# Optimization experiments

Hardware: AMD Instinct MI355X
Metric: run time of the kernel (lower is better)

Reference implementation:

```python
import jax, jax.numpy as jnp
from jax import lax
import numpy as np

H = 128          # hidden_size
E = 300          # embed_dim
V = 100000       # vocab size


def lstm_dir(x, Wih, Whh, b, reverse):
    # x: (B,T,D); Wih: (4H,D); Whh: (4H,H); b: (4H,) (bih+bhh combined)
    B, T, _ = x.shape
    h_dim = Whh.shape[1]
    xg = jnp.einsum('btd,gd->btg', x, Wih) + b  # precompute input gates (B,T,4H)

    def step(carry, xt):
        h, c = carry
        gates = xt + h @ Whh.T
        i, f, g, o = jnp.split(gates, 4, axis=-1)  # PyTorch gate order i,f,g,o
        i = jax.nn.sigmoid(i); f = jax.nn.sigmoid(f)
        g = jnp.tanh(g);       o = jax.nn.sigmoid(o)
        c = f * c + i * g
        h = o * jnp.tanh(c)
        return (h, c), h

    init = (jnp.zeros((B, h_dim), x.dtype), jnp.zeros((B, h_dim), x.dtype))
    _, hs = lax.scan(step, init, jnp.swapaxes(xg, 0, 1), reverse=reverse)
    return jnp.swapaxes(hs, 0, 1)  # (B,T,H)


def bilstm(x, Wih, Whh, b):
    # stacked params: Wih (2,4H,D), Whh (2,4H,H), b (2,4H); dir 0 fwd, dir 1 bwd
    fwd = lstm_dir(x, Wih[0], Whh[0], b[0], False)
    bwd = lstm_dir(x, Wih[1], Whh[1], b[1], True)
    return jnp.concatenate([fwd, bwd], axis=-1)  # (B,T,2H)


def _lstm_params(key, in_dim, h):
    ks = jax.random.split(key, 3)
    s = 1.0 / np.sqrt(h)
    return (jax.random.uniform(ks[0], (2, 4 * h, in_dim), jnp.float32, -s, s),
            jax.random.uniform(ks[1], (2, 4 * h, h), jnp.float32, -s, s),
            jax.random.uniform(ks[2], (2, 4 * h), jnp.float32, -s, s))


def setup_inputs() -> dict:
    key = jax.random.key(0)
    ks = jax.random.split(key, 16)
    inp = {}
    inp['p'] = jax.random.randint(ks[0], (64, 512), 0, V)
    inp['q'] = jax.random.randint(ks[1], (64, 64), 0, V)
    inp['emb'] = jax.random.normal(ks[2], (V, E), jnp.float32) * 0.1
    for name, in_dim, k in [('qenc', E, ks[3]), ('penc', E, ks[4]),
                            ('m1', 8 * H, ks[5]), ('m2', 2 * H, ks[6]),
                            ('out', 2 * H, ks[7])]:
        Wih, Whh, b = _lstm_params(k, in_dim, H)
        inp[name + '_Wih'] = Wih; inp[name + '_Whh'] = Whh; inp[name + '_b'] = b
    inp['att_wc'] = jax.random.normal(ks[8], (2 * H,), jnp.float32) * 0.05
    inp['att_wq'] = jax.random.normal(ks[9], (2 * H,), jnp.float32) * 0.05
    inp['att_wcq'] = jax.random.normal(ks[10], (2 * H,), jnp.float32) * 0.05
    inp['att_b'] = jnp.zeros((), jnp.float32)
    inp['p1_wg'] = jax.random.normal(ks[11], (8 * H,), jnp.float32) * 0.05
    inp['p1_wm'] = jax.random.normal(ks[12], (2 * H,), jnp.float32) * 0.05
    inp['p1_b'] = jnp.zeros((), jnp.float32)
    inp['p2_wg'] = jax.random.normal(ks[13], (8 * H,), jnp.float32) * 0.05
    inp['p2_wm'] = jax.random.normal(ks[14], (2 * H,), jnp.float32) * 0.05
    inp['p2_b'] = jnp.zeros((), jnp.float32)
    return inp


def reference(p, q, emb,
              qenc_Wih, qenc_Whh, qenc_b,
              penc_Wih, penc_Whh, penc_b,
              m1_Wih, m1_Whh, m1_b,
              m2_Wih, m2_Whh, m2_b,
              out_Wih, out_Whh, out_b,
              att_wc, att_wq, att_wcq, att_b,
              p1_wg, p1_wm, p1_b, p2_wg, p2_wm, p2_b):
    q_emb = emb[q]                      # (B,Q,E)
    p_emb = emb[p]                      # (B,C,E)
    qo = bilstm(q_emb, qenc_Wih, qenc_Whh, qenc_b)   # (B,Q,2H)
    co = bilstm(p_emb, penc_Wih, penc_Whh, penc_b)   # (B,C,2H)

    # trilinear similarity (fused form of the original per-q_len loop)
    s = (jnp.einsum('bcd,d->bc', co, att_wc)[:, :, None]
         + jnp.einsum('bqd,d->bq', qo, att_wq)[:, None, :]
         + jnp.einsum('bcd,bqd->bcq', co * att_wcq, qo)
         + att_b)                       # (B,C,Q)
    a = jax.nn.softmax(s, axis=2)
    c2q = jnp.einsum('bcq,bqd->bcd', a, qo)
    bw = jax.nn.softmax(jnp.max(s, axis=2), axis=1)   # (B,C)
    q2c = jnp.einsum('bc,bcd->bd', bw, co)[:, None, :]  # (B,1,2H)
    g = jnp.concatenate([co, c2q, co * c2q, co * q2c], axis=-1)  # (B,C,8H)

    m = bilstm(bilstm(g, m1_Wih, m1_Whh, m1_b), m2_Wih, m2_Whh, m2_b)  # (B,C,2H)
    m2 = bilstm(m, out_Wih, out_Whh, out_b)

    p1_logit = g @ p1_wg + m @ p1_wm + p1_b    # (B,C)
    p2_logit = g @ p2_wg + m2 @ p2_wm + p2_b
    valid = (p != 0)
    p1 = jax.nn.softmax(jnp.where(valid, p1_logit, -jnp.inf), axis=1)
    p2 = jax.nn.softmax(jnp.where(valid, p2_logit, -jnp.inf), axis=1)
    return p1, p2
```

## Files before the change

kernel.cpp:

```cpp
#include <hip/hip_runtime.h>
#include <math.h>
#include <stdint.h>

#define HD    128
#define GATES 512
#define BB    64
#define CL    512
#define QL    64

#define TM 128
#define TN 128
#define TK 32
#define ASTR 40

typedef __attribute__((ext_vector_type(8))) short short8_t;
typedef __attribute__((ext_vector_type(4))) short short4_t;
typedef __attribute__((ext_vector_type(4))) float f32x4;
typedef __attribute__((ext_vector_type(2))) float f32x2;

__device__ __forceinline__ float fast_sigmoid(float x) {
    float e = __builtin_amdgcn_exp2f(-1.44269504f * x);
    return __builtin_amdgcn_rcpf(1.f + e);
}
__device__ __forceinline__ float fast_tanh(float x) {
    float e = __builtin_amdgcn_exp2f(2.88539008f * x);
    float r = __builtin_amdgcn_rcpf(e + 1.f);
    return 1.f - 2.f * r;
}
__device__ __forceinline__ float quad_sum(float v) {
    int y = __builtin_amdgcn_mov_dpp(__float_as_int(v), 0xB1, 0xF, 0xF, 0);
    float s = v + __int_as_float(y);
    int z = __builtin_amdgcn_mov_dpp(__float_as_int(s), 0x4E, 0xF, 0xF, 0);
    return s + __int_as_float(z);
}
#define HPOS(e) ((e) + (((e) >> 5) << 2))

__global__ __launch_bounds__(256)
void splitW_k(const float* __restrict__ W, ushort* __restrict__ P, int K, int Ksp)
{
    int idx = blockIdx.x * 256 + threadIdx.x;
    int per_row = Ksp >> 2;
    int total = 1024 * per_row;
    if (idx >= total) return;
    int row = idx / per_row;
    int c4  = (idx - row * per_row) * 4;

    short4_t o1, o2, o3;
#pragma unroll
    for (int e = 0; e < 4; ++e) {
        int k = c4 + e;
        float x = (k < K) ? W[(size_t)row * K + k] : 0.f;
        uint32_t u1 = __float_as_uint(x) & 0xffff0000u;
        float r1 = x - __uint_as_float(u1);
        uint32_t u2 = __float_as_uint(r1) & 0xffff0000u;
        float r2 = r1 - __uint_as_float(u2);
        uint32_t u3 = __float_as_uint(r2) & 0xffff0000u;
        o1[e] = (short)(u1 >> 16);
        o2[e] = (short)(u2 >> 16);
        o3[e] = (short)(u3 >> 16);
    }
    size_t base = (size_t)row * Ksp + c4;
    size_t ps = (size_t)1024 * Ksp;
    *reinterpret_cast<short4_t*>(&P[base]) = o1;
    *reinterpret_cast<short4_t*>(&P[ps + base]) = o2;
    *reinterpret_cast<short4_t*>(&P[2 * ps + base]) = o3;
}

__global__ __launch_bounds__(256)
void gemm_bf16x3(const float* __restrict__ A, const int* __restrict__ gidx,
                 const ushort* __restrict__ Wpl, const float* __restrict__ bias,
                 float* __restrict__ C, int M, int K, int Ksp)
{
    const int n0   = (blockIdx.x & 3) * TN / 1;
    const int dir  = blockIdx.x >> 2;
    const int m0   = blockIdx.y * TM;
    const int tid  = threadIdx.x;
    const int lane = tid & 63;
    const int wid  = tid >> 6;
    const int wm   = (wid >> 1) * 64;
    const int wn   = (wid & 1) * 64;

    __shared__ __align__(16) ushort As[3][TM * ASTR];
    __shared__ __align__(16) ushort Bs[3][TN * TK];

    const int ar = tid >> 3;
    const int ac = (tid & 7) * 4;

    size_t arow[4];
#pragma unroll
    for (int r = 0; r < 4; ++r) {
        int m = m0 + ar + r * 32;
        arow[r] = gidx ? (size_t)gidx[m] : (size_t)m;
    }

    f32x4 acc[4][4];
#pragma unroll
    for (int i = 0; i < 4; ++i)
#pragma unroll
        for (int j = 0; j < 4; ++j) acc[i][j] = (f32x4)0.f;

    const size_t wps    = (size_t)1024 * Ksp;
    const size_t wdbase = (size_t)dir * 512 * Ksp;

    for (int k0 = 0; k0 < Ksp; k0 += TK) {
#pragma unroll
        for (int r = 0; r < 4; ++r) {
            float4 v = make_float4(0.f, 0.f, 0.f, 0.f);
            if (k0 + ac < K) v = *(const float4*)(A + arow[r] * K + k0 + ac);
            float xs[4] = {v.x, v.y, v.z, v.w};
            short4_t o1, o2, o3;
#pragma unroll
            for (int e = 0; e < 4; ++e) {
                uint32_t u1 = __float_as_uint(xs[e]) & 0xffff0000u;
                float r1 = xs[e] - __uint_as_float(u1);
                uint32_t u2 = __float_as_uint(r1) & 0xffff0000u;
                float r2 = r1 - __uint_as_float(u2);
                uint32_t u3 = __float_as_uint(r2) & 0xffff0000u;
                o1[e] = (short)(u1 >> 16);
                o2[e] = (short)(u2 >> 16);
                o3[e] = (short)(u3 >> 16);
            }
            int wb = (ar + r * 32) * ASTR + ac;
            *reinterpret_cast<short4_t*>(&As[0][wb]) = o1;
            *reinterpret_cast<short4_t*>(&As[1][wb]) = o2;
            *reinterpret_cast<short4_t*>(&As[2][wb]) = o3;
        }
#pragma unroll
        for (int t = 0; t < 6; ++t) {
            int chunk = wid * 6 + t;
            int pl = chunk >> 3;
            int ch = chunk & 7;
            int rrow = ch * 16 + (lane >> 2);
            int ksw  = ((lane & 3) ^ ((rrow >> 1) & 3)) * 8;
            const ushort* src = Wpl + (size_t)pl * wps + wdbase +
                                (size_t)(n0 + rrow) * Ksp + k0 + ksw;
            ushort* dst = &Bs[pl][ch * 512];
            __builtin_amdgcn_global_load_lds(
                reinterpret_cast<const __attribute__((address_space(1))) void*>(
                    reinterpret_cast<uintptr_t>(src)),
                reinterpret_cast<__attribute__((address_space(3))) void*>(
                    reinterpret_cast<uintptr_t>(dst)),
                16, 0, 0);
        }
        __syncthreads();

        const int koff = (lane >> 4) * 8;
        short8_t bf0[4], bf1[4], bf2[4];
#pragma unroll
        for (int j = 0; j < 4; ++j) {
            int nrow = wn + j * 16 + (lane & 15);
            int ks = (((lane >> 4) ^ ((nrow >> 1) & 3)) * 8);
            bf0[j] = *reinterpret_cast<const short8_t*>(&Bs[0][nrow * TK + ks]);
            bf1[j] = *reinterpret_cast<const short8_t*>(&Bs[1][nrow * TK + ks]);
            bf2[j] = *reinterpret_cast<const short8_t*>(&Bs[2][nrow * TK + ks]);
        }
#pragma unroll
        for (int i = 0; i < 4; ++i) {
            int mrow = wm + i * 16 + (lane & 15);
            short8_t a1 = *reinterpret_cast<const short8_t*>(&As[0][mrow * ASTR + koff]);
            short8_t a2 = *reinterpret_cast<const short8_t*>(&As[1][mrow * ASTR + koff]);
            short8_t a3 = *reinterpret_cast<const short8_t*>(&As[2][mrow * ASTR + koff]);
#pragma unroll
            for (int j = 0; j < 4; ++j) {
                f32x4 c = acc[i][j];
                c = __builtin_amdgcn_mfma_f32_16x16x32_bf16(a1, bf0[j], c, 0, 0, 0);
                c = __builtin_amdgcn_mfma_f32_16x16x32_bf16(a1, bf1[j], c, 0, 0, 0);
                c = __builtin_amdgcn_mfma_f32_16x16x32_bf16(a2, bf0[j], c, 0, 0, 0);
                c = __builtin_amdgcn_mfma_f32_16x16x32_bf16(a2, bf1[j], c, 0, 0, 0);
                c = __builtin_amdgcn_mfma_f32_16x16x32_bf16(a1, bf2[j], c, 0, 0, 0);
                c = __builtin_amdgcn_mfma_f32_16x16x32_bf16(a3, bf0[j], c, 0, 0, 0);
                acc[i][j] = c;
            }
        }
        __syncthreads();
    }

    float* Cd = C + (size_t)dir * M * 512;
#pragma unroll
    for (int j = 0; j < 4; ++j) {
        int col = n0 + wn + j * 16 + (lane & 15);
        float bv = bias[dir * 512 + col];
#pragma unroll
        for (int i = 0; i < 4; ++i) {
            int rbase = m0 + wm + i * 16 + ((lane >> 4) << 2);
#pragma unroll
            for (int r = 0; r < 4; ++r)
                Cd[(size_t)(rbase + r) * 512 + col] = acc[i][j][r] + bv;
        }
    }
}

__global__ __launch_bounds__(512) __attribute__((amdgpu_waves_per_eu(2, 2)))
void lstm_dpp(const float* __restrict__ xgP, const float* __restrict__ WhhP,
              float* __restrict__ hoP, int TP,
              const float* __restrict__ xgQ, const float* __restrict__ WhhQ,
              float* __restrict__ hoQ, int TQ)
{
    const int b    = blockIdx.x;
    const int dir  = blockIdx.y;
    const int tid  = threadIdx.x;
    const int l    = tid & 63;
    const int w    = tid >> 6;
    const int u    = w * 16 + (l >> 2);
    const int s    = l & 3;

    const float* xg; const float* Whh; float* ho; int T;
    if (blockIdx.z == 0) { xg = xgP; Whh = WhhP; ho = hoP; T = TP; }
    else                 { xg = xgQ; Whh = WhhQ; ho = hoQ; T = TQ; }

    const float* xgd = xg + (size_t)dir * BB * T * GATES;

    f32x2 wv2[4][16];
#pragma unroll
    for (int g = 0; g < 4; ++g) {
        const float* wr = Whh + ((size_t)dir * GATES + g * 128 + u) * HD + s * 32;
#pragma unroll
        for (int j = 0; j < 8; ++j) {
            float4 t4 = *(const float4*)(wr + j * 4);
            wv2[g][2 * j]     = f32x2{t4.x, t4.y};
            wv2[g][2 * j + 1] = f32x2{t4.z, t4.w};
        }
    }

    __shared__ __align__(16) float hs[2][140];

    if (tid < 140) { hs[0][tid] = 0.f; }
    float c = 0.f;

    int t = dir ? (T - 1) : 0;
    const int dt = dir ? -1 : 1;

    float xc[4], xn[4];
#pragma unroll
    for (int g = 0; g < 4; ++g)
        xc[g] = xgd[((size_t)b * T + t) * GATES + g * 128 + u];

    const int rdbase = HPOS(s * 32);
    __syncthreads();

    for (int step = 0; step < T; ++step) {
        const int tn = t + dt;
        const int rbuf = step & 1, wbuf = rbuf ^ 1;

        if (step + 1 < T) {
#pragma unroll
            for (int g = 0; g < 4; ++g)
                xn[g] = xgd[((size_t)b * T + tn) * GATES + g * 128 + u];
        }

        f32x2 p0 = {0.f, 0.f}, p1 = {0.f, 0.f}, p2 = {0.f, 0.f}, p3 = {0.f, 0.f};
#pragma unroll
        for (int j = 0; j < 8; ++j) {
            float4 h4 = *(const float4*)&hs[rbuf][rdbase + j * 4];
            f32x2 hl = {h4.x, h4.y}, hh = {h4.z, h4.w};
            p0 = __builtin_elementwise_fma(wv2[0][2 * j], hl, p0);
            p1 = __builtin_elementwise_fma(wv2[1][2 * j], hl, p1);
            p2 = __builtin_elementwise_fma(wv2[2][2 * j], hl, p2);
            p3 = __builtin_elementwise_fma(wv2[3][2 * j], hl, p3);
            p0 = __builtin_elementwise_fma(wv2[0][2 * j + 1], hh, p0);
            p1 = __builtin_elementwise_fma(wv2[1][2 * j + 1], hh, p1);
            p2 = __builtin_elementwise_fma(wv2[2][2 * j + 1], hh, p2);
            p3 = __builtin_elementwise_fma(wv2[3][2 * j + 1], hh, p3);
        }
        float pre0 = quad_sum(p0.x + p0.y) + xc[0];
        float pre1 = quad_sum(p1.x + p1.y) + xc[1];
        float pre2 = quad_sum(p2.x + p2.y) + xc[2];
        float pre3 = quad_sum(p3.x + p3.y) + xc[3];

        float ig = fast_sigmoid(pre0);
        float fg = fast_sigmoid(pre1);
        float gg = fast_tanh(pre2);
        float og = fast_sigmoid(pre3);
        c = fg * c + ig * gg;
        float h = og * fast_tanh(c);

        if (s == 0) {
            hs[wbuf][HPOS(u)] = h;
            ho[((size_t)b * T + t) * 256 + dir * HD + u] = h;
        }
        __syncthreads();

#pragma unroll
        for (int g = 0; g < 4; ++g) xc[g] = xn[g];
        t = tn;
    }
}

__global__ void rowdot(const float* __restrict__ X, const float* __restrict__ w,
                       float* __restrict__ out, int N, int D)
{
    int gw   = (int)((blockIdx.x * blockDim.x + threadIdx.x) >> 6);
    int lane = threadIdx.x & 63;
    if (gw >= N) return;
    const float* xp = X + (size_t)gw * D;
    float s = 0.f;
    for (int d = lane; d < D; d += 64) s += xp[d] * w[d];
#pragma unroll
    for (int off = 32; off; off >>= 1) s += __shfl_down(s, off);
    if (lane == 0) out[gw] = s;
}

__global__ __launch_bounds__(256)
void att_s(const float* __restrict__ co, const float* __restrict__ qo,
           const float* __restrict__ cw, const float* __restrict__ qw,
           const float* __restrict__ wcq, const float* __restrict__ attb,
           float* __restrict__ s)
{
    int b  = blockIdx.x;
    int c0 = blockIdx.y * 64;
    int tid = threadIdx.x;
    int tq = tid & 15, trc = tid >> 4;
    int cbase = c0 + trc * 4, qbase = tq * 4;

    float acc[4][4];
#pragma unroll
    for (int i = 0; i < 4; ++i)
#pragma unroll
        for (int j = 0; j < 4; ++j) acc[i][j] = 0.f;

    for (int d = 0; d < 256; d += 4) {
        float4 wv = *(const float4*)&wcq[d];
        float4 cv[4], qv[4];
#pragma unroll
        for (int i = 0; i < 4; ++i) {
            float4 v = *(const float4*)&co[((size_t)b * CL + cbase + i) * 256 + d];
            cv[i].x = v.x * wv.x; cv[i].y = v.y * wv.y;
            cv[i].z = v.z * wv.z; cv[i].w = v.w * wv.w;
        }
#pragma unroll
        for (int j = 0; j < 4; ++j)
            qv[j] = *(const float4*)&qo[((size_t)b * QL + qbase + j) * 256 + d];
#pragma unroll
        for (int i = 0; i < 4; ++i)
#pragma unroll
            for (int j = 0; j < 4; ++j)
                acc[i][j] += cv[i].x * qv[j].x + cv[i].y * qv[j].y +
                             cv[i].z * qv[j].z + cv[i].w * qv[j].w;
    }
    float ab = attb[0];
#pragma unroll
    for (int i = 0; i < 4; ++i) {
        float cwv = cw[b * CL + cbase + i];
#pragma unroll
        for (int j = 0; j < 4; ++j) {
            s[((size_t)b * CL + cbase + i) * QL + qbase + j] =
                acc[i][j] + cwv + qw[b * QL + qbase + j] + ab;
        }
    }
}

__global__ void softmax_q(float* __restrict__ s, float* __restrict__ smax)
{
    int gw   = (int)((blockIdx.x * blockDim.x + threadIdx.x) >> 6);
    int lane = threadIdx.x & 63;
    float v = s[(size_t)gw * QL + lane];
    float mx = v;
#pragma unroll
    for (int off = 32; off; off >>= 1) mx = fmaxf(mx, __shfl_xor(mx, off));
    float e = expf(v - mx);
    float sm = e;
#pragma unroll
    for (int off = 32; off; off >>= 1) sm += __shfl_xor(sm, off);
    s[(size_t)gw * QL + lane] = e / sm;
    if (lane == 0) smax[gw] = mx;
}

__global__ __launch_bounds__(512)
void bw_k(const float* __restrict__ smax, float* __restrict__ bw)
{
    int b = blockIdx.x, c = threadIdx.x;
    int lane = c & 63, wid = c >> 6;
    __shared__ float red[8];
    float v = smax[b * CL + c];
    float mx = v;
#pragma unroll
    for (int off = 32; off; off >>= 1) mx = fmaxf(mx, __shfl_xor(mx, off));
    if (lane == 0) red[wid] = mx;
    __syncthreads();
    float bm = red[0];
#pragma unroll
    for (int w = 1; w < 8; ++w) bm = fmaxf(bm, red[w]);
    float e = expf(v - bm);
    float sm = e;
#pragma unroll
    for (int off = 32; off; off >>= 1) sm += __shfl_xor(sm, off);
    __syncthreads();
    if (lane == 0) red[wid] = sm;
    __syncthreads();
    float ts = 0.f;
#pragma unroll
    for (int w = 0; w < 8; ++w) ts += red[w];
    bw[b * CL + c] = e / ts;
}

__global__ __launch_bounds__(256)
void q2c_k(const float* __restrict__ bw, const float* __restrict__ co,
           float* __restrict__ q2c)
{
    int b = blockIdx.x, d = threadIdx.x;
    float acc = 0.f;
    for (int c = 0; c < CL; ++c)
        acc += bw[b * CL + c] * co[((size_t)b * CL + c) * 256 + d];
    q2c[b * 256 + d] = acc;
}

__global__ __launch_bounds__(256)
void c2q_g(const float* __restrict__ a, const float* __restrict__ qo,
           const float* __restrict__ co, const float* __restrict__ q2c,
           float* __restrict__ g)
{
    int b  = blockIdx.x;
    int c  = blockIdx.y * 64 + (threadIdx.x >> 2);
    int gq = threadIdx.x & 3;

    float4 acc[16];
#pragma unroll
    for (int jj = 0; jj < 16; ++jj) acc[jj] = make_float4(0.f, 0.f, 0.f, 0.f);

    const float* ar = a + ((size_t)b * CL + c) * QL;
    for (int q = 0; q < QL; ++q) {
        float av = ar[q];
        const float* qr = qo + ((size_t)b * QL + q) * 256;
#pragma unroll
        for (int jj = 0; jj < 16; ++jj) {
            float4 qv = *(const float4*)&qr[4 * gq + 16 * jj];
            acc[jj].x += av * qv.x; acc[jj].y += av * qv.y;
            acc[jj].z += av * qv.z; acc[jj].w += av * qv.w;
        }
    }
    size_t gbase = ((size_t)b * CL + c) * 1024;
    const float* corow = co + ((size_t)b * CL + c) * 256;
    const float* q2cr  = q2c + b * 256;
#pragma unroll
    for (int jj = 0; jj < 16; ++jj) {
        int d = 4 * gq + 16 * jj;
        float4 cv = *(const float4*)&corow[d];
        float4 qc = *(const float4*)&q2cr[d];
        float4 cq = acc[jj];
        *(float4*)&g[gbase + d] = cv;
        *(float4*)&g[gbase + 256 + d] = cq;
        float4 t;
        t.x = cv.x * cq.x; t.y = cv.y * cq.y; t.z = cv.z * cq.z; t.w = cv.w * cq.w;
        *(float4*)&g[gbase + 512 + d] = t;
        t.x = cv.x * qc.x; t.y = cv.y * qc.y; t.z = cv.z * qc.z; t.w = cv.w * qc.w;
        *(float4*)&g[gbase + 768 + d] = t;
    }
}

__global__ void logits_k(const float* __restrict__ g, const float* __restrict__ m,
                         const float* __restrict__ m2o,
                         const float* __restrict__ p1wg, const float* __restrict__ p1wm,
                         const float* __restrict__ p1b,
                         const float* __restrict__ p2wg, const float* __restrict__ p2wm,
                         const float* __restrict__ p2b,
                         float* __restrict__ lp1, float* __restrict__ lp2)
{
    int row  = (int)((blockIdx.x * blockDim.x + threadIdx.x) >> 6);
    int lane = threadIdx.x & 63;
    const float* gr = g + (size_t)row * 1024;
    float s1 = 0.f, s2 = 0.f;
    for (int d = lane; d < 1024; d += 64) {
        float gv = gr[d];
        s1 += gv * p1wg[d];
        s2 += gv * p2wg[d];
    }
    const float* mr  = m   + (size_t)row * 256;
    const float* m2r = m2o + (size_t)row * 256;
    for (int d = lane; d < 256; d += 64) {
        s1 += mr[d] * p1wm[d];
        s2 += m2r[d] * p2wm[d];
    }
#pragma unroll
    for (int off = 32; off; off >>= 1) {
        s1 += __shfl_down(s1, off);
        s2 += __shfl_down(s2, off);
    }
    if (lane == 0) {
        lp1[row] = s1 + p1b[0];
        lp2[row] = s2 + p2b[0];
    }
}

__global__ __launch_bounds__(512)
void masked_softmax(const float* __restrict__ lp1, const float* __restrict__ lp2,
                    const int* __restrict__ p, float* __restrict__ out)
{
    int b = blockIdx.x, c = threadIdx.x;
    int lane = c & 63, wid = c >> 6;
    const float* lp = blockIdx.y ? lp2 : lp1;
    float* o = out + (size_t)blockIdx.y * BB * CL;

    __shared__ float red[8];
    float v = (p[b * CL + c] != 0) ? lp[b * CL + c] : -INFINITY;
    float mx = v;
#pragma unroll
    for (int off = 32; off; off >>= 1) mx = fmaxf(mx, __shfl_xor(mx, off));
    if (lane == 0) red[wid] = mx;
    __syncthreads();
    float bm = red[0];
#pragma unroll
    for (int w = 1; w < 8; ++w) bm = fmaxf(bm, red[w]);
    float e = expf(v - bm);
    float sm = e;
#pragma unroll
    for (int off = 32; off; off >>= 1) sm += __shfl_xor(sm, off);
    __syncthreads();
    if (lane == 0) red[wid] = sm;
    __syncthreads();
    float ts = 0.f;
#pragma unroll
    for (int w = 0; w < 8; ++w) ts += red[w];
    o[b * CL + c] = e / ts;
}

extern "C" void kernel_launch(void* const* d_in, const int* in_sizes, int n_in,
                              void* d_out, int out_size, void* d_ws, size_t ws_size,
                              hipStream_t stream)
{
    const int*   p        = (const int*)d_in[0];
    const int*   q        = (const int*)d_in[1];
    const float* emb      = (const float*)d_in[2];
    const float* qenc_Wih = (const float*)d_in[3];
    const float* qenc_Whh = (const float*)d_in[4];
    const float* qenc_b   = (const float*)d_in[5];
    const float* penc_Wih = (const float*)d_in[6];
    const float* penc_Whh = (const float*)d_in[7];
    const float* penc_b   = (const float*)d_in[8];
    const float* m1_Wih   = (const float*)d_in[9];
    const float* m1_Whh   = (const float*)d_in[10];
    const float* m1_b     = (const float*)d_in[11];
    const float* m2_Wih   = (const float*)d_in[12];
    const float* m2_Whh   = (const float*)d_in[13];
    const float* m2_b     = (const float*)d_in[14];
    const float* out_Wih  = (const float*)d_in[15];
    const float* out_Whh  = (const float*)d_in[16];
    const float* out_b    = (const float*)d_in[17];
    const float* att_wc   = (const float*)d_in[18];
    const float* att_wq   = (const float*)d_in[19];
    const float* att_wcq  = (const float*)d_in[20];
    const float* att_b    = (const float*)d_in[21];
    const float* p1_wg    = (const float*)d_in[22];
    const float* p1_wm    = (const float*)d_in[23];
    const float* p1_b     = (const float*)d_in[24];
    const float* p2_wg    = (const float*)d_in[25];
    const float* p2_wm    = (const float*)d_in[26];
    const float* p2_b     = (const float*)d_in[27];

    float* ws = (float*)d_ws;
    size_t off = 0;
    auto alloc = [&](size_t n) { float* r = ws + off; off += n; return r; };
    auto allocU = [&](size_t nsh) { ushort* r = (ushort*)(ws + off); off += (nsh + 1) / 2; return r; };

    const size_t NC = (size_t)BB * CL;
    const size_t NQ = (size_t)BB * QL;

    float* xgA  = alloc(2 * NC * GATES);
    float* gbuf = alloc(NC * 1024);
    float* xgQ  = gbuf;
    float* co   = alloc(NC * 256);
    float* qo   = alloc(NQ * 256);
    float* sbuf = alloc(NC * QL);
    float* cw   = alloc(NC);
    float* qw   = alloc(NQ);
    float* smax = alloc(NC);
    float* bw   = alloc(NC);
    float* q2c  = alloc((size_t)BB * 256);
    float* mmid = alloc(NC * 256);
    float* mbuf = alloc(NC * 256);
    float* m2o  = alloc(NC * 256);
    float* lp1  = alloc(NC);
    float* lp2  = alloc(NC);
    ushort* WqP  = allocU((size_t)3 * 1024 * 320);
    ushort* WpP  = allocU((size_t)3 * 1024 * 320);
    ushort* Wm1P = allocU((size_t)3 * 1024 * 1024);
    ushort* Wm2P = allocU((size_t)3 * 1024 * 256);
    ushort* WoP  = allocU((size_t)3 * 1024 * 256);
    (void)ws_size; (void)in_sizes; (void)n_in; (void)out_size;

    splitW_k<<<dim3(1024 * 80 / 256), 256, 0, stream>>>(qenc_Wih, WqP, 300, 320);
    splitW_k<<<dim3(1024 * 80 / 256), 256, 0, stream>>>(penc_Wih, WpP, 300, 320);
    splitW_k<<<dim3(1024 * 256 / 256), 256, 0, stream>>>(m1_Wih, Wm1P, 1024, 1024);
    splitW_k<<<dim3(1024 * 64 / 256), 256, 0, stream>>>(m2_Wih, Wm2P, 256, 256);
    splitW_k<<<dim3(1024 * 64 / 256), 256, 0, stream>>>(out_Wih, WoP, 256, 256);

    gemm_bf16x3<<<dim3(8, (int)(NQ / TM)), 256, 0, stream>>>(emb, q, WqP, qenc_b, xgQ, (int)NQ, 300, 320);
    gemm_bf16x3<<<dim3(8, (int)(NC / TM)), 256, 0, stream>>>(emb, p, WpP, penc_b, xgA, (int)NC, 300, 320);
    lstm_dpp<<<dim3(BB, 2, 2), 512, 0, stream>>>(xgA, penc_Whh, co, CL,
                                                 xgQ, qenc_Whh, qo, QL);

    rowdot<<<dim3((int)(NC * 64 / 256)), 256, 0, stream>>>(co, att_wc, cw, (int)NC, 256);
    rowdot<<<dim3((int)(NQ * 64 / 256)), 256, 0, stream>>>(qo, att_wq, qw, (int)NQ, 256);
    att_s<<<dim3(BB, CL / 64), 256, 0, stream>>>(co, qo, cw, qw, att_wcq, att_b, sbuf);
    softmax_q<<<dim3((int)(NC * 64 / 256)), 256, 0, stream>>>(sbuf, smax);
    bw_k<<<dim3(BB), 512, 0, stream>>>(smax, bw);
    q2c_k<<<dim3(BB), 256, 0, stream>>>(bw, co, q2c);
    c2q_g<<<dim3(BB, CL / 64), 256, 0, stream>>>(sbuf, qo, co, q2c, gbuf);

    gemm_bf16x3<<<dim3(8, (int)(NC / TM)), 256, 0, stream>>>(gbuf, nullptr, Wm1P, m1_b, xgA, (int)NC, 1024, 1024);
    lstm_dpp<<<dim3(BB, 2, 1), 512, 0, stream>>>(xgA, m1_Whh, mmid, CL,
                                                 xgA, m1_Whh, mmid, CL);
    gemm_bf16x3<<<dim3(8, (int)(NC / TM)), 256, 0, stream>>>(mmid, nullptr, Wm2P, m2_b, xgA, (int)NC, 256, 256);
    lstm_dpp<<<dim3(BB, 2, 1), 512, 0, stream>>>(xgA, m2_Whh, mbuf, CL,
                                                 xgA, m2_Whh, mbuf, CL);
    gemm_bf16x3<<<dim3(8, (int)(NC / TM)), 256, 0, stream>>>(mbuf, nullptr, WoP, out_b, xgA, (int)NC, 256, 256);
    lstm_dpp<<<dim3(BB, 2, 1), 512, 0, stream>>>(xgA, out_Whh, m2o, CL,
                                                 xgA, out_Whh, m2o, CL);

    logits_k<<<dim3((int)(NC * 64 / 256)), 256, 0, stream>>>(gbuf, mbuf, m2o,
        p1_wg, p1_wm, p1_b, p2_wg, p2_wm, p2_b, lp1, lp2);
    masked_softmax<<<dim3(BB, 2), 512, 0, stream>>>(lp1, lp2, p, (float*)d_out);
}
```

Measured before the change: 2.771 ms.

## Double-buffer weight tiles and load A fragments directly into registers

Restructures the bf16x3 input-projection GEMM so that B weight tiles are double-buffered in LDS, with the next tile prefetched asynchronously while the current one is consumed. The A operand no longer goes through LDS: each lane loads its MFMA fragment straight from global memory and splits it into three bf16 parts in registers. A launch-bounds occupancy hint of 3 blocks is also added. The aim is to overlap global loads with MFMA work and remove the A-tile LDS traffic, at the cost of redundant A global reads across waves and more register pressure.

Result: slower. 3.154 ms (+13.9%).

```diff
diff --git a/kernel.cpp b/kernel.cpp
--- a/kernel.cpp
+++ b/kernel.cpp
@@ -11,7 +11,6 @@
 #define TM 128
 #define TN 128
 #define TK 32
-#define ASTR 40
 
 typedef __attribute__((ext_vector_type(8))) short short8_t;
 typedef __attribute__((ext_vector_type(4))) short short4_t;
@@ -66,12 +65,12 @@
     *reinterpret_cast<short4_t*>(&P[2 * ps + base]) = o3;
 }
 
-__global__ __launch_bounds__(256)
+__global__ __launch_bounds__(256, 3)
 void gemm_bf16x3(const float* __restrict__ A, const int* __restrict__ gidx,
                  const ushort* __restrict__ Wpl, const float* __restrict__ bias,
                  float* __restrict__ C, int M, int K, int Ksp)
 {
-    const int n0   = (blockIdx.x & 3) * TN / 1;
+    const int n0   = (blockIdx.x & 3) * TN;
     const int dir  = blockIdx.x >> 2;
     const int m0   = blockIdx.y * TM;
     const int tid  = threadIdx.x;
@@ -80,18 +79,15 @@
     const int wm   = (wid >> 1) * 64;
     const int wn   = (wid & 1) * 64;
 
-    __shared__ __align__(16) ushort As[3][TM * ASTR];
-    __shared__ __align__(16) ushort Bs[3][TN * TK];
-
-    const int ar = tid >> 3;
-    const int ac = (tid & 7) * 4;
+    __shared__ __align__(16) ushort Bs[2][3][TN * TK];
 
     size_t arow[4];
 #pragma unroll
-    for (int r = 0; r < 4; ++r) {
-        int m = m0 + ar + r * 32;
-        arow[r] = gidx ? (size_t)gidx[m] : (size_t)m;
-    }
+    for (int i = 0; i < 4; ++i) {
+        int m = m0 + wm + i * 16 + (lane & 15);
+        arow[i] = gidx ? (size_t)gidx[m] : (size_t)m;
+    }
+    const int koffE = (lane >> 4) * 8;
 
     f32x4 acc[4][4];
 #pragma unroll
@@ -102,64 +98,104 @@
     const size_t wps    = (size_t)1024 * Ksp;
     const size_t wdbase = (size_t)dir * 512 * Ksp;
 
-    for (int k0 = 0; k0 < Ksp; k0 += TK) {
-#pragma unroll
-        for (int r = 0; r < 4; ++r) {
-            float4 v = make_float4(0.f, 0.f, 0.f, 0.f);
-            if (k0 + ac < K) v = *(const float4*)(A + arow[r] * K + k0 + ac);
-            float xs[4] = {v.x, v.y, v.z, v.w};
-            short4_t o1, o2, o3;
-#pragma unroll
-            for (int e = 0; e < 4; ++e) {
+    const int s_pl   = (wid * 6) / 8;
+    (void)s_pl;
+
+    const int nt = Ksp / TK;
+
+#pragma unroll
+    for (int t = 0; t < 6; ++t) {
+        int chunk = wid * 6 + t;
+        int pl = chunk >> 3;
+        int ch = chunk & 7;
+        int rrow = ch * 16 + (lane >> 2);
+        int ksw  = ((lane & 3) ^ ((rrow >> 1) & 3)) * 8;
+        const ushort* src = Wpl + (size_t)pl * wps + wdbase +
+                            (size_t)(n0 + rrow) * Ksp + 0 + ksw;
+        ushort* dst = &Bs[0][pl][ch * 512];
+        __builtin_amdgcn_global_load_lds(
+            reinterpret_cast<const __attribute__((address_space(1))) void*>(
+                reinterpret_cast<uintptr_t>(src)),
+            reinterpret_cast<__attribute__((address_space(3))) void*>(
+                reinterpret_cast<uintptr_t>(dst)),
+            16, 0, 0);
+    }
+    __syncthreads();
+
+    int buf = 0;
+    for (int kt = 0; kt < nt; ++kt) {
+        const int k0 = kt * TK;
+
+        if (kt + 1 < nt) {
+#pragma unroll
+            for (int t = 0; t < 6; ++t) {
+                int chunk = wid * 6 + t;
+                int pl = chunk >> 3;
+                int ch = chunk & 7;
+                int rrow = ch * 16 + (lane >> 2);
+                int ksw  = ((lane & 3) ^ ((rrow >> 1) & 3)) * 8;
+                const ushort* src = Wpl + (size_t)pl * wps + wdbase +
+                                    (size_t)(n0 + rrow) * Ksp + (k0 + TK) + ksw;
+                ushort* dst = &Bs[buf ^ 1][pl][ch * 512];
+                __builtin_amdgcn_global_load_lds(
+                    reinterpret_cast<const __attribute__((address_space(1))) void*>(
+                        reinterpret_cast<uintptr_t>(src)),
+                    reinterpret_cast<__attribute__((address_space(3))) void*>(
+                        reinterpret_cast<uintptr_t>(dst)),
+                    16, 0, 0);
+            }
+        }
+
+        float4 ra[4][2];
+        const bool tail = (k0 + TK > K);
+        if (!tail) {
+#pragma unroll
+            for (int i = 0; i < 4; ++i) {
+                const float* ap = A + arow[i] * K + k0 + koffE;
+                ra[i][0] = *(const float4*)ap;
+                ra[i][1] = *(const float4*)(ap + 4);
+            }
+        } else {
+#pragma unroll
+            for (int i = 0; i < 4; ++i) {
+                const float* ap = A + arow[i] * K;
+                float tmp[8];
+#pragma unroll
+                for (int e = 0; e < 8; ++e) {
+                    int k = k0 + koffE + e;
+                    tmp[e] = (k < K) ? ap[k] : 0.f;
+                }
+                ra[i][0] = make_float4(tmp[0], tmp[1], tmp[2], tmp[3]);
+                ra[i][1] = make_float4(tmp[4], tmp[5], tmp[6], tmp[7]);
+            }
+        }
+
+        short8_t bf0[4], bf1[4], bf2[4];
+#pragma unroll
+        for (int j = 0; j < 4; ++j) {
+            int nrow = wn + j * 16 + (lane & 15);
+            int ks = (((lane >> 4) ^ ((nrow >> 1) & 3)) * 8);
+            bf0[j] = *reinterpret_cast<const short8_t*>(&Bs[buf][0][nrow * TK + ks]);
+            bf1[j] = *reinterpret_cast<const short8_t*>(&Bs[buf][1][nrow * TK + ks]);
+            bf2[j] = *reinterpret_cast<const short8_t*>(&Bs[buf][2][nrow * TK + ks]);
+        }
+
+#pragma unroll
+        for (int i = 0; i < 4; ++i) {
+            float xs[8] = {ra[i][0].x, ra[i][0].y, ra[i][0].z, ra[i][0].w,
+                           ra[i][1].x, ra[i][1].y, ra[i][1].z, ra[i][1].w};
+            short8_t a1, a2, a3;
+#pragma unroll
+            for (int e = 0; e < 8; ++e) {
                 uint32_t u1 = __float_as_uint(xs[e]) & 0xffff0000u;
                 float r1 = xs[e] - __uint_as_float(u1);
                 uint32_t u2 = __float_as_uint(r1) & 0xffff0000u;
                 float r2 = r1 - __uint_as_float(u2);
                 uint32_t u3 = __float_as_uint(r2) & 0xffff0000u;
-                o1[e] = (short)(u1 >> 16);
-                o2[e] = (short)(u2 >> 16);
-                o3[e] = (short)(u3 >> 16);
+                a1[e] = (short)(u1 >> 16);
+                a2[e] = (short)(u2 >> 16);
+                a3[e] = (short)(u3 >> 16);
             }
-            int wb = (ar + r * 32) * ASTR + ac;
-            *reinterpret_cast<short4_t*>(&As[0][wb]) = o1;
-            *reinterpret_cast<short4_t*>(&As[1][wb]) = o2;
-            *reinterpret_cast<short4_t*>(&As[2][wb]) = o3;
-        }
-#pragma unroll
-        for (int t = 0; t < 6; ++t) {
-            int chunk = wid * 6 + t;
-            int pl = chunk >> 3;
-            int ch = chunk & 7;
-            int rrow = ch * 16 + (lane >> 2);
-            int ksw  = ((lane & 3) ^ ((rrow >> 1) & 3)) * 8;
-            const ushort* src = Wpl + (size_t)pl * wps + wdbase +
-                                (size_t)(n0 + rrow) * Ksp + k0 + ksw;
-            ushort* dst = &Bs[pl][ch * 512];
-            __builtin_amdgcn_global_load_lds(
-                reinterpret_cast<const __attribute__((address_space(1))) void*>(
-                    reinterpret_cast<uintptr_t>(src)),
-                reinterpret_cast<__attribute__((address_space(3))) void*>(
-                    reinterpret_cast<uintptr_t>(dst)),
-                16, 0, 0);
-        }
-        __syncthreads();
-
-        const int koff = (lane >> 4) * 8;
-        short8_t bf0[4], bf1[4], bf2[4];
-#pragma unroll
-        for (int j = 0; j < 4; ++j) {
-            int nrow = wn + j * 16 + (lane & 15);
-            int ks = (((lane >> 4) ^ ((nrow >> 1) & 3)) * 8);
-            bf0[j] = *reinterpret_cast<const short8_t*>(&Bs[0][nrow * TK + ks]);
-            bf1[j] = *reinterpret_cast<const short8_t*>(&Bs[1][nrow * TK + ks]);
-            bf2[j] = *reinterpret_cast<const short8_t*>(&Bs[2][nrow * TK + ks]);
-        }
-#pragma unroll
-        for (int i = 0; i < 4; ++i) {
-            int mrow = wm + i * 16 + (lane & 15);
-            short8_t a1 = *reinterpret_cast<const short8_t*>(&As[0][mrow * ASTR + koff]);
-            short8_t a2 = *reinterpret_cast<const short8_t*>(&As[1][mrow * ASTR + koff]);
-            short8_t a3 = *reinterpret_cast<const short8_t*>(&As[2][mrow * ASTR + koff]);
 #pragma unroll
             for (int j = 0; j < 4; ++j) {
                 f32x4 c = acc[i][j];
@@ -173,6 +209,7 @@
             }
         }
         __syncthreads();
+        buf ^= 1;
     }
 
     float* Cd = C + (size_t)dir * M * 512;
```

## Double-buffer GEMM tiles and split fp32 A into bf16 planes at fragment load

Applied to the files above, without the earlier changes.

The input-projection GEMM now keeps two LDS buffers for both A and B tiles and prefetches the next K-tile while computing the current one. Only one barrier per iteration remains. A is staged as raw fp32 in a swizzled layout, and the three-way bf16 split is done per thread right after reading the MFMA fragment, instead of during staging. It also sets launch bounds to a minimum of 2 blocks per CU. The aim is to hide global-load latency behind MFMA work, at the cost of more LDS, more register pressure, and redundant split arithmetic across the waves that read the same A rows.

New measurement: 2.740 ms. No clear change (-1.1%).

```diff
diff --git a/kernel.cpp b/kernel.cpp
--- a/kernel.cpp
+++ b/kernel.cpp
@@ -11,7 +11,6 @@
 #define TM 128
 #define TN 128
 #define TK 32
-#define ASTR 40
 
 typedef __attribute__((ext_vector_type(8))) short short8_t;
 typedef __attribute__((ext_vector_type(4))) short short4_t;
@@ -66,12 +65,12 @@
     *reinterpret_cast<short4_t*>(&P[2 * ps + base]) = o3;
 }
 
-__global__ __launch_bounds__(256)
+__global__ __launch_bounds__(256, 2)
 void gemm_bf16x3(const float* __restrict__ A, const int* __restrict__ gidx,
                  const ushort* __restrict__ Wpl, const float* __restrict__ bias,
                  float* __restrict__ C, int M, int K, int Ksp)
 {
-    const int n0   = (blockIdx.x & 3) * TN / 1;
+    const int n0   = (blockIdx.x & 3) * TN;
     const int dir  = blockIdx.x >> 2;
     const int m0   = blockIdx.y * TM;
     const int tid  = threadIdx.x;
@@ -80,18 +79,19 @@
     const int wm   = (wid >> 1) * 64;
     const int wn   = (wid & 1) * 64;
 
-    __shared__ __align__(16) ushort As[3][TM * ASTR];
-    __shared__ __align__(16) ushort Bs[3][TN * TK];
-
-    const int ar = tid >> 3;
-    const int ac = (tid & 7) * 4;
-
-    size_t arow[4];
+    __shared__ __align__(16) float  Asf[2][TM * TK];
+    __shared__ __align__(16) ushort Bs[2][3][TN * TK];
+
+    const int srow = tid >> 3;
+    const int scol = tid & 7;
+    size_t sArow[4];
 #pragma unroll
     for (int r = 0; r < 4; ++r) {
-        int m = m0 + ar + r * 32;
-        arow[r] = gidx ? (size_t)gidx[m] : (size_t)m;
-    }
+        int m = m0 + srow + r * 32;
+        sArow[r] = gidx ? (size_t)gidx[m] : (size_t)m;
+    }
+
+    const int s0 = (lane >> 4) * 2;
 
     f32x4 acc[4][4];
 #pragma unroll
@@ -101,30 +101,9 @@
 
     const size_t wps    = (size_t)1024 * Ksp;
     const size_t wdbase = (size_t)dir * 512 * Ksp;
-
-    for (int k0 = 0; k0 < Ksp; k0 += TK) {
-#pragma unroll
-        for (int r = 0; r < 4; ++r) {
-            float4 v = make_float4(0.f, 0.f, 0.f, 0.f);
-            if (k0 + ac < K) v = *(const float4*)(A + arow[r] * K + k0 + ac);
-            float xs[4] = {v.x, v.y, v.z, v.w};
-            short4_t o1, o2, o3;
-#pragma unroll
-            for (int e = 0; e < 4; ++e) {
-                uint32_t u1 = __float_as_uint(xs[e]) & 0xffff0000u;
-                float r1 = xs[e] - __uint_as_float(u1);
-                uint32_t u2 = __float_as_uint(r1) & 0xffff0000u;
-                float r2 = r1 - __uint_as_float(u2);
-                uint32_t u3 = __float_as_uint(r2) & 0xffff0000u;
-                o1[e] = (short)(u1 >> 16);
-                o2[e] = (short)(u2 >> 16);
-                o3[e] = (short)(u3 >> 16);
-            }
-            int wb = (ar + r * 32) * ASTR + ac;
-            *reinterpret_cast<short4_t*>(&As[0][wb]) = o1;
-            *reinterpret_cast<short4_t*>(&As[1][wb]) = o2;
-            *reinterpret_cast<short4_t*>(&As[2][wb]) = o3;
-        }
+    const int nt = Ksp / TK;
+
+    auto stageB = [&](int k0, int bufb) {
 #pragma unroll
         for (int t = 0; t < 6; ++t) {
             int chunk = wid * 6 + t;
@@ -134,7 +113,7 @@
             int ksw  = ((lane & 3) ^ ((rrow >> 1) & 3)) * 8;
             const ushort* src = Wpl + (size_t)pl * wps + wdbase +
                                 (size_t)(n0 + rrow) * Ksp + k0 + ksw;
-            ushort* dst = &Bs[pl][ch * 512];
+            ushort* dst = &Bs[bufb][pl][ch * 512];
             __builtin_amdgcn_global_load_lds(
                 reinterpret_cast<const __attribute__((address_space(1))) void*>(
                     reinterpret_cast<uintptr_t>(src)),
@@ -142,24 +121,67 @@
                     reinterpret_cast<uintptr_t>(dst)),
                 16, 0, 0);
         }
-        __syncthreads();
-
-        const int koff = (lane >> 4) * 8;
+    };
+    auto stageA = [&](int k0, int bufb) {
+#pragma unroll
+        for (int r = 0; r < 4; ++r) {
+            int row = srow + r * 32;
+            int kf  = k0 + scol * 4;
+            float4 v;
+            if (kf + 4 <= K) {
+                v = *(const float4*)(A + sArow[r] * K + kf);
+            } else {
+                const float* ap = A + sArow[r] * K;
+                v.x = (kf     < K) ? ap[kf]     : 0.f;
+                v.y = (kf + 1 < K) ? ap[kf + 1] : 0.f;
+                v.z = (kf + 2 < K) ? ap[kf + 2] : 0.f;
+                v.w = (kf + 3 < K) ? ap[kf + 3] : 0.f;
+            }
+            int sw = scol ^ (row & 7);
+            *(float4*)&Asf[bufb][row * TK + sw * 4] = v;
+        }
+    };
+
+    stageB(0, 0);
+    stageA(0, 0);
+    __syncthreads();
+
+    int buf = 0;
+    for (int kt = 0; kt < nt; ++kt) {
+        if (kt + 1 < nt) {
+            stageB((kt + 1) * TK, buf ^ 1);
+            stageA((kt + 1) * TK, buf ^ 1);
+        }
+
         short8_t bf0[4], bf1[4], bf2[4];
 #pragma unroll
         for (int j = 0; j < 4; ++j) {
             int nrow = wn + j * 16 + (lane & 15);
             int ks = (((lane >> 4) ^ ((nrow >> 1) & 3)) * 8);
-            bf0[j] = *reinterpret_cast<const short8_t*>(&Bs[0][nrow * TK + ks]);
-            bf1[j] = *reinterpret_cast<const short8_t*>(&Bs[1][nrow * TK + ks]);
-            bf2[j] = *reinterpret_cast<const short8_t*>(&Bs[2][nrow * TK + ks]);
-        }
+            bf0[j] = *reinterpret_cast<const short8_t*>(&Bs[buf][0][nrow * TK + ks]);
+            bf1[j] = *reinterpret_cast<const short8_t*>(&Bs[buf][1][nrow * TK + ks]);
+            bf2[j] = *reinterpret_cast<const short8_t*>(&Bs[buf][2][nrow * TK + ks]);
+        }
+
 #pragma unroll
         for (int i = 0; i < 4; ++i) {
             int mrow = wm + i * 16 + (lane & 15);
-            short8_t a1 = *reinterpret_cast<const short8_t*>(&As[0][mrow * ASTR + koff]);
-            short8_t a2 = *reinterpret_cast<const short8_t*>(&As[1][mrow * ASTR + koff]);
-            short8_t a3 = *reinterpret_cast<const short8_t*>(&As[2][mrow * ASTR + koff]);
+            int rx = mrow & 7;
+            float4 fa = *(const float4*)&Asf[buf][mrow * TK + ((s0)     ^ rx) * 4];
+            float4 fb = *(const float4*)&Asf[buf][mrow * TK + ((s0 + 1) ^ rx) * 4];
+            float xs[8] = {fa.x, fa.y, fa.z, fa.w, fb.x, fb.y, fb.z, fb.w};
+            short8_t a1, a2, a3;
+#pragma unroll
+            for (int e = 0; e < 8; ++e) {
+                uint32_t u1 = __float_as_uint(xs[e]) & 0xffff0000u;
+                float r1 = xs[e] - __uint_as_float(u1);
+                uint32_t u2 = __float_as_uint(r1) & 0xffff0000u;
+                float r2 = r1 - __uint_as_float(u2);
+                uint32_t u3 = __float_as_uint(r2) & 0xffff0000u;
+                a1[e] = (short)(u1 >> 16);
+                a2[e] = (short)(u2 >> 16);
+                a3[e] = (short)(u3 >> 16);
+            }
 #pragma unroll
             for (int j = 0; j < 4; ++j) {
                 f32x4 c = acc[i][j];
@@ -173,6 +195,7 @@
             }
         }
         __syncthreads();
+        buf ^= 1;
     }
 
     float* Cd = C + (size_t)dir * M * 512;
```
